# Performance work log

Hardware: AMD Instinct MI355X
Metric: run time of the kernel (lower is better)

The kernel has to match this reference:

```python
import jax, jax.numpy as jnp
import numpy as np

NUM_HEADS = 2
POOL_K = 256
REPEAT = 20


def setup_inputs() -> dict:
    key = jax.random.key(0)
    k1, k2, k3 = jax.random.split(key, 3)
    C = 6144
    d = C // NUM_HEADS                      # 3072
    N = REPEAT * (d // POOL_K)              # 240, required by Pq add
    x = jax.random.normal(k1, (N, C), dtype=jnp.float32)
    w_qkv = jax.random.normal(k2, (3 * C, C), dtype=jnp.float32) * 0.02
    w_proj = jax.random.normal(k3, (C, C), dtype=jnp.float32) * 0.02
    b_proj = jnp.zeros((C,), dtype=jnp.float32)
    return {"x": x, "w_qkv": w_qkv, "w_proj": w_proj, "b_proj": b_proj}


def reference(x, w_qkv, w_proj, b_proj):
    N, C = x.shape
    H = NUM_HEADS
    d = C // H
    scale = d ** -0.5
    # qkv: (N, 3C) -> (N, 3, H, d) -> (3, H, N, d)
    qkv = (x @ w_qkv.T).reshape(N, 3, H, d).transpose(1, 2, 0, 3)
    q, k, v = qkv[0], qkv[1], qkv[2]        # each (H, N, d)
    # MaxPool1d(256) over last dim, then tile x20 along last dim -> (H, N, N)
    Pq = q.reshape(H, N, d // POOL_K, POOL_K).max(axis=-1)
    Pq = jnp.tile(Pq, (1, 1, REPEAT))       # (H, N, N)
    attn = jnp.einsum('hnd,hmd->hnm', q, k) * scale + 0.1 * Pq
    attn = jax.nn.softmax(attn, axis=-1)
    out = jnp.einsum('hnm,hmd->hnd', attn, v)    # (H, N, d)
    out = out.transpose(1, 0, 2).reshape(N, C)
    return out @ w_proj.T + b_proj
```

## Files before the change

kernel.cpp:

```cpp
#include <hip/hip_runtime.h>
#include <hip/hip_bf16.h>

#define NN 240
#define CC 6144
#define DD 3072
#define C3 18432
#define HH 2

typedef __attribute__((ext_vector_type(8))) short bf16x8;
typedef __attribute__((ext_vector_type(4))) float f32x4;
typedef unsigned short ushort_t;

static __device__ __forceinline__ unsigned short f2bf(float f) {
    __hip_bfloat16 h = __float2bfloat16(f);
    return __builtin_bit_cast(unsigned short, h);
}

#define GLDS16(g, l) __builtin_amdgcn_global_load_lds( \
    (const __attribute__((address_space(1))) void*)(g), \
    (__attribute__((address_space(3))) void*)(l), 16, 0, 0)

__global__ __launch_bounds__(512, 4)
void gemm_v6(const ushort_t* __restrict__ Ab, int lda, long long sAz,
             const float* __restrict__ B, int ldb, long long sBz,
             const float* __restrict__ bias,
             float* __restrict__ C0, long long sC0z,
             float* __restrict__ CP, long long sCPz,
             int ldc, int N, int Kc, int KS,
             ushort_t* __restrict__ Qb) {
    __shared__ ushort_t sA[2][256 * 64];
    __shared__ ushort_t sB[2][32 * 64];

    const int zc = blockIdx.z;
    const int z = zc / KS, kc = zc % KS;
    const ushort_t* Abase = Ab + (size_t)z * sAz + (size_t)kc * Kc;
    const float*    Bbase = B  + (size_t)z * sBz + (size_t)kc * Kc;
    float* Cw = (kc == 0) ? (C0 + (size_t)z * sC0z)
                          : (CP + (size_t)(z * (KS - 1) + kc - 1) * sCPz);

    const int n0 = blockIdx.x * 32;
    const int tid = threadIdx.x, lane = tid & 63, wid = tid >> 6;
    const int wm = wid >> 1, wn = wid & 1;
    const int l16 = lane & 15, lk = lane >> 4;

    const int arow = wid * 32 + (lane >> 3);
    const ushort_t* ap = Abase + (size_t)arow * lda
                         + ((lane & 7) ^ ((lane >> 3) & 7)) * 8;

    const int brow = tid >> 4, bq = tid & 15;
    int brow_c = n0 + brow; if (brow_c > N - 1) brow_c = N - 1;
    const float* bp = Bbase + (size_t)brow_c * ldb + bq * 4;
    const int bws = brow * 128 + ((((bq >> 1) ^ (brow & 7)) << 4) + (bq & 1) * 8);

    const int nt = Kc / 64;
    f32x4 acc[4] = {};

    auto ISSUE_A = [&](int t, int par) {
        const ushort_t* a = ap + (size_t)t * 64;
#pragma unroll
        for (int i = 0; i < 4; ++i)
            GLDS16(a + (size_t)i * 8 * lda, &sA[par][(wid * 4 + i) * 512]);
    };
    auto LOAD_B = [&](int t) {
        return *(const float4*)(bp + (size_t)t * 64);
    };
    auto WRITE_B = [&](int par, float4 g) {
        ushort4 u;
        u.x = f2bf(g.x); u.y = f2bf(g.y); u.z = f2bf(g.z); u.w = f2bf(g.w);
        *(ushort4*)(reinterpret_cast<char*>(&sB[par][0]) + bws) = u;
    };
    auto MFMA_PH = [&](int cur) {
        const char* As = (const char*)sA[cur];
        const char* Bs = (const char*)sB[cur];
#pragma unroll
        for (int ks = 0; ks < 2; ++ks) {
            bf16x8 af[4], bf1;
#pragma unroll
            for (int mt = 0; mt < 4; ++mt) {
                int row = wm * 64 + mt * 16 + l16;
                int boff = row * 128 + (((ks * 4 + lk) * 16) ^ ((row & 7) << 4));
                af[mt] = *(const bf16x8*)(As + boff);
            }
            {
                int row = wn * 16 + l16;
                int boff = row * 128 + (((ks * 4 + lk) * 16) ^ ((row & 7) << 4));
                bf1 = *(const bf16x8*)(Bs + boff);
            }
            __builtin_amdgcn_s_setprio(1);
#pragma unroll
            for (int mt = 0; mt < 4; ++mt)
                acc[mt] = __builtin_amdgcn_mfma_f32_16x16x32_bf16(
                    af[mt], bf1, acc[mt], 0, 0, 0);
            __builtin_amdgcn_s_setprio(0);
        }
    };

    float4 e, o;

    ISSUE_A(0, 0);
    e = LOAD_B(0);
    o = (nt > 1) ? LOAD_B(1) : e;
    asm volatile("s_waitcnt vmcnt(1)" ::: "memory");
    __builtin_amdgcn_sched_barrier(0);
    WRITE_B(0, e);
    asm volatile("s_waitcnt lgkmcnt(0)" ::: "memory");
    __builtin_amdgcn_s_barrier();

    auto STEP = [&](int t, float4& w, float4& r) {
        int ta = t + 1 < nt ? t + 1 : nt - 1;
        int tb = t + 2 < nt ? t + 2 : nt - 1;
        ISSUE_A(ta, (t + 1) & 1);
        w = LOAD_B(tb);
        __builtin_amdgcn_sched_barrier(0);
        asm volatile("s_waitcnt vmcnt(6)" ::: "memory");
        __builtin_amdgcn_sched_barrier(0);
        MFMA_PH(t & 1);
        __builtin_amdgcn_sched_barrier(0);
        asm volatile("s_waitcnt vmcnt(5)" ::: "memory");
        __builtin_amdgcn_sched_barrier(0);
        WRITE_B((t + 1) & 1, r);
        asm volatile("s_waitcnt lgkmcnt(0)" ::: "memory");
        __builtin_amdgcn_s_barrier();
    };

    for (int t = 0; t < nt; t += 2) {
        STEP(t,     e, o);
        STEP(t + 1, o, e);
    }

#pragma unroll
    for (int mt = 0; mt < 4; ++mt) {
#pragma unroll
        for (int j = 0; j < 4; ++j) {
            int grow = wm * 64 + mt * 16 + lk * 4 + j;
            if (grow < NN) {
                int gcol = n0 + wn * 16 + l16;
                if (gcol < N) {
                    float v = acc[mt][j];
                    if (kc == 0 && bias) v += bias[gcol];
                    Cw[(size_t)grow * ldc + gcol] = v;
                    if (Qb && gcol < CC)
                        Qb[(size_t)grow * CC + gcol] = f2bf(v);
                }
            }
        }
    }
}

__global__ __launch_bounds__(256)
void convert_kernel(const float* __restrict__ x, ushort_t* __restrict__ xb) {
    int id = blockIdx.x * 256 + threadIdx.x;
    int row = id / 768, c8 = id % 768;
    bf16x8 o = {};
    if (row < NN) {
        const float* p = x + (size_t)row * CC + c8 * 8;
        float4 a = *(const float4*)p, b = *(const float4*)(p + 4);
        o[0] = (short)f2bf(a.x); o[1] = (short)f2bf(a.y);
        o[2] = (short)f2bf(a.z); o[3] = (short)f2bf(a.w);
        o[4] = (short)f2bf(b.x); o[5] = (short)f2bf(b.y);
        o[6] = (short)f2bf(b.z); o[7] = (short)f2bf(b.w);
    }
    *(bf16x8*)(xb + (size_t)row * CC + c8 * 8) = o;
}

__global__ __launch_bounds__(256)
void reduce_proj(float4* __restrict__ o4, const float4* __restrict__ p4,
                 long long s4) {
    int i = blockIdx.x * 256 + threadIdx.x;
    float4 a = o4[i];
#pragma unroll
    for (int k = 0; k < 2; ++k) {
        float4 b = p4[(size_t)k * s4 + i];
        a.x += b.x; a.y += b.y; a.z += b.z; a.w += b.w;
    }
    o4[i] = a;
}

__global__ __launch_bounds__(256)
void qmax_kernel(const float* __restrict__ qkv, float* __restrict__ qmax) {
    int idx = blockIdx.x * 4 + (threadIdx.x >> 6);
    int lane = threadIdx.x & 63;
    int c = idx % 12;
    int r = idx / 12;
    int n = r % NN, h = r / NN;
    const float* p = qkv + (size_t)n * C3 + h * DD + c * 256 + lane * 4;
    float4 f = *(const float4*)p;
    float m = fmaxf(fmaxf(f.x, f.y), fmaxf(f.z, f.w));
#pragma unroll
    for (int off = 32; off >= 1; off >>= 1)
        m = fmaxf(m, __shfl_xor(m, off));
    if (lane == 0) qmax[idx] = m;
}

__global__ __launch_bounds__(256)
void softmax_kernel(float* __restrict__ attn, const float* __restrict__ gpart,
                    int ksm1, const float* __restrict__ qmax) {
    int r = blockIdx.x * 4 + (threadIdx.x >> 6);
    int lane = threadIdx.x & 63;
    int z = r / NN, n = r % NN;
    float* row = attn + (size_t)r * NN;
    const float* qm = qmax + r * 12;
    const float scale = 0.0180421959f;
    float v[4];
    float mx = -1e30f;
#pragma unroll
    for (int i = 0; i < 4; ++i) {
        int m = lane + 64 * i;
        v[i] = -1e30f;
        if (m < NN) {
            float s = row[m];
            for (int kc = 0; kc < ksm1; ++kc)
                s += gpart[(size_t)(z * ksm1 + kc) * (NN * NN)
                           + (size_t)n * NN + m];
            v[i] = s * scale + 0.1f * qm[m % 12];
        }
        mx = fmaxf(mx, v[i]);
    }
#pragma unroll
    for (int off = 32; off >= 1; off >>= 1)
        mx = fmaxf(mx, __shfl_xor(mx, off));
    float s = 0.f;
#pragma unroll
    for (int i = 0; i < 4; ++i) {
        v[i] = __expf(v[i] - mx);
        s += v[i];
    }
#pragma unroll
    for (int off = 32; off >= 1; off >>= 1)
        s += __shfl_xor(s, off);
    float inv = 1.0f / s;
#pragma unroll
    for (int i = 0; i < 4; ++i) {
        int m = lane + 64 * i;
        if (m < NN) row[m] = v[i] * inv;
    }
}

__global__ __launch_bounds__(256)
void pv_kernel(const float* __restrict__ attn, const float* __restrict__ qkv,
               ushort_t* __restrict__ preb) {
    const int h = blockIdx.z;
    const int n0 = blockIdx.y * 16;
    const int dd0 = blockIdx.x * 256;
    __shared__ float s_attn[16 * NN];
    for (int i = threadIdx.x; i < 16 * NN; i += 256)
        s_attn[i] = attn[(size_t)h * NN * NN + (n0 + i / NN) * NN + (i % NN)];
    __syncthreads();

    const float* vp = qkv + 2 * CC + h * DD + dd0 + threadIdx.x;
    float acc[16] = {};
    for (int m = 0; m < NN; m += 4) {
        float v0 = vp[(size_t)(m + 0) * C3];
        float v1 = vp[(size_t)(m + 1) * C3];
        float v2 = vp[(size_t)(m + 2) * C3];
        float v3 = vp[(size_t)(m + 3) * C3];
#pragma unroll
        for (int i = 0; i < 16; ++i) {
            float4 a = *(const float4*)&s_attn[i * NN + m];
            acc[i] += a.x * v0 + a.y * v1 + a.z * v2 + a.w * v3;
        }
    }
#pragma unroll
    for (int i = 0; i < 16; ++i)
        preb[(size_t)(n0 + i) * CC + h * DD + dd0 + threadIdx.x] =
            f2bf(acc[i]);
}

extern "C" void kernel_launch(void* const* d_in, const int* in_sizes, int n_in,
                              void* d_out, int out_size, void* d_ws, size_t ws_size,
                              hipStream_t stream) {
    const float* x      = (const float*)d_in[0];
    const float* w_qkv  = (const float*)d_in[1];
    const float* w_proj = (const float*)d_in[2];
    const float* b_proj = (const float*)d_in[3];
    float* out = (float*)d_out;

    const size_t f_qkv  = (size_t)NN * C3;
    const size_t f_attn = (size_t)HH * NN * NN;
    const size_t f_qmax = (size_t)HH * NN * 12;
    float* qkv   = (float*)d_ws;
    float* attn  = qkv + f_qkv;
    float* qmaxb = attn + f_attn;
    ushort_t* xb   = (ushort_t*)(qmaxb + f_qmax);
    ushort_t* qb   = xb + (size_t)256 * CC;
    ushort_t* preb = qb + (size_t)256 * CC;
    float* gpart = (float*)(preb + (size_t)256 * CC);

    convert_kernel<<<768, 256, 0, stream>>>(x, xb);

    gemm_v6<<<dim3(C3 / 32, 1, 1), 512, 0, stream>>>(
        xb, CC, 0LL, w_qkv, CC, 0LL, nullptr,
        qkv, 0LL, gpart, 0LL,
        C3, C3, CC, 1, qb);

    qmax_kernel<<<1440, 256, 0, stream>>>(qkv, qmaxb);

    gemm_v6<<<dim3(8, 1, HH * 24), 512, 0, stream>>>(
        qb, CC, (long long)DD,
        qkv + CC, C3, (long long)DD, nullptr,
        attn, (long long)(NN * NN), gpart, (long long)(NN * NN),
        NN, NN, DD / 24, 24, nullptr);

    softmax_kernel<<<120, 256, 0, stream>>>(attn, gpart, 23, qmaxb);

    pv_kernel<<<dim3(12, 15, HH), 256, 0, stream>>>(attn, qkv, preb);

    gemm_v6<<<dim3(CC / 32, 1, 3), 512, 0, stream>>>(
        preb, CC, 0LL, w_proj, CC, 0LL, b_proj,
        out, 0LL, gpart, (long long)((size_t)NN * CC),
        CC, CC, CC / 3, 3, nullptr);
    reduce_proj<<<1440, 256, 0, stream>>>((float4*)out, (const float4*)gpart,
        (long long)((size_t)NN * CC / 4));
}
```

Measured before the change: 424.9 us.

## Keep B operand in registers and widen GEMM tile to 64 columns

Replaces the 512-thread GEMM, which staged the fp32 weight tile through LDS after bf16 conversion, with a 256-thread kernel. Each wave now loads its own 16 weight columns straight into registers, converts them, and feeds them as the MFMA B fragment. Each wave covers all 256 rows (16 accumulators), so the A tile in LDS is reused across four waves per 64-column block. This removes the LDS writes and reads for B and one barrier per step, but raises register pressure, lowers occupancy, halves the grid and leaves an uncoalesced-ish strided B load.

```diff
diff --git a/kernel.cpp b/kernel.cpp
--- a/kernel.cpp
+++ b/kernel.cpp
@@ -20,8 +20,8 @@
     (const __attribute__((address_space(1))) void*)(g), \
     (__attribute__((address_space(3))) void*)(l), 16, 0, 0)
 
-__global__ __launch_bounds__(512, 4)
-void gemm_v6(const ushort_t* __restrict__ Ab, int lda, long long sAz,
+__global__ __launch_bounds__(256, 2)
+void gemm_rs(const ushort_t* __restrict__ Ab, int lda, long long sAz,
              const float* __restrict__ B, int ldb, long long sBz,
              const float* __restrict__ bias,
              float* __restrict__ C0, long long sC0z,
@@ -29,7 +29,6 @@
              int ldc, int N, int Kc, int KS,
              ushort_t* __restrict__ Qb) {
     __shared__ ushort_t sA[2][256 * 64];
-    __shared__ ushort_t sB[2][32 * 64];
 
     const int zc = blockIdx.z;
     const int z = zc / KS, kc = zc % KS;
@@ -38,103 +37,88 @@
     float* Cw = (kc == 0) ? (C0 + (size_t)z * sC0z)
                           : (CP + (size_t)(z * (KS - 1) + kc - 1) * sCPz);
 
-    const int n0 = blockIdx.x * 32;
+    const int n0 = blockIdx.x * 64;
     const int tid = threadIdx.x, lane = tid & 63, wid = tid >> 6;
-    const int wm = wid >> 1, wn = wid & 1;
     const int l16 = lane & 15, lk = lane >> 4;
 
-    const int arow = wid * 32 + (lane >> 3);
-    const ushort_t* ap = Abase + (size_t)arow * lda
+    const ushort_t* ap = Abase + (size_t)(wid * 64 + (lane >> 3)) * lda
                          + ((lane & 7) ^ ((lane >> 3) & 7)) * 8;
 
-    const int brow = tid >> 4, bq = tid & 15;
-    int brow_c = n0 + brow; if (brow_c > N - 1) brow_c = N - 1;
-    const float* bp = Bbase + (size_t)brow_c * ldb + bq * 4;
-    const int bws = brow * 128 + ((((bq >> 1) ^ (brow & 7)) << 4) + (bq & 1) * 8);
+    int colc = n0 + wid * 16 + l16; if (colc > N - 1) colc = N - 1;
+    const float* bp = Bbase + (size_t)colc * ldb + lk * 8;
 
     const int nt = Kc / 64;
-    f32x4 acc[4] = {};
-
-    auto ISSUE_A = [&](int t, int par) {
-        const ushort_t* a = ap + (size_t)t * 64;
-#pragma unroll
-        for (int i = 0; i < 4; ++i)
-            GLDS16(a + (size_t)i * 8 * lda, &sA[par][(wid * 4 + i) * 512]);
-    };
-    auto LOAD_B = [&](int t) {
-        return *(const float4*)(bp + (size_t)t * 64);
-    };
-    auto WRITE_B = [&](int par, float4 g) {
-        ushort4 u;
-        u.x = f2bf(g.x); u.y = f2bf(g.y); u.z = f2bf(g.z); u.w = f2bf(g.w);
-        *(ushort4*)(reinterpret_cast<char*>(&sB[par][0]) + bws) = u;
-    };
-    auto MFMA_PH = [&](int cur) {
-        const char* As = (const char*)sA[cur];
-        const char* Bs = (const char*)sB[cur];
-#pragma unroll
-        for (int ks = 0; ks < 2; ++ks) {
-            bf16x8 af[4], bf1;
-#pragma unroll
-            for (int mt = 0; mt < 4; ++mt) {
-                int row = wm * 64 + mt * 16 + l16;
-                int boff = row * 128 + (((ks * 4 + lk) * 16) ^ ((row & 7) << 4));
-                af[mt] = *(const bf16x8*)(As + boff);
-            }
-            {
-                int row = wn * 16 + l16;
-                int boff = row * 128 + (((ks * 4 + lk) * 16) ^ ((row & 7) << 4));
-                bf1 = *(const bf16x8*)(Bs + boff);
-            }
-            __builtin_amdgcn_s_setprio(1);
-#pragma unroll
-            for (int mt = 0; mt < 4; ++mt)
-                acc[mt] = __builtin_amdgcn_mfma_f32_16x16x32_bf16(
-                    af[mt], bf1, acc[mt], 0, 0, 0);
-            __builtin_amdgcn_s_setprio(0);
-        }
-    };
-
-    float4 e, o;
+    f32x4 acc[16] = {};
+
+    auto ISSUE_A = [&](int u, int par) {
+        const ushort_t* a = ap + (size_t)u * 64;
+        ushort_t* d = &sA[par][wid * 8 * 512];
+#pragma unroll
+        for (int i = 0; i < 8; ++i)
+            GLDS16(a + (size_t)i * 8 * lda, d + i * 512);
+    };
+    auto LOAD_B4 = [&](int u, float4& b0, float4& b1, float4& b2, float4& b3) {
+        const float* p = bp + (size_t)u * 64;
+        b0 = *(const float4*)p;
+        b1 = *(const float4*)(p + 4);
+        b2 = *(const float4*)(p + 32);
+        b3 = *(const float4*)(p + 36);
+    };
+    auto PHASE = [&](int buf, int ph, float4 g0, float4 g1) {
+        bf16x8 bfr;
+        bfr[0] = (short)f2bf(g0.x); bfr[1] = (short)f2bf(g0.y);
+        bfr[2] = (short)f2bf(g0.z); bfr[3] = (short)f2bf(g0.w);
+        bfr[4] = (short)f2bf(g1.x); bfr[5] = (short)f2bf(g1.y);
+        bfr[6] = (short)f2bf(g1.z); bfr[7] = (short)f2bf(g1.w);
+        const char* As = (const char*)sA[buf];
+        __builtin_amdgcn_s_setprio(1);
+#pragma unroll
+        for (int mt = 0; mt < 16; ++mt) {
+            int row = mt * 16 + l16;
+            int boff = row * 128 + (((ph * 4 + lk) * 16) ^ ((row & 7) << 4));
+            bf16x8 af = *(const bf16x8*)(As + boff);
+            acc[mt] = __builtin_amdgcn_mfma_f32_16x16x32_bf16(
+                af, bfr, acc[mt], 0, 0, 0);
+        }
+        __builtin_amdgcn_s_setprio(0);
+    };
+
+    float4 e0, e1, e2, e3, o0, o1, o2, o3;
 
     ISSUE_A(0, 0);
-    e = LOAD_B(0);
-    o = (nt > 1) ? LOAD_B(1) : e;
-    asm volatile("s_waitcnt vmcnt(1)" ::: "memory");
+    LOAD_B4(0, e0, e1, e2, e3);
+    LOAD_B4(nt > 1 ? 1 : 0, o0, o1, o2, o3);
     __builtin_amdgcn_sched_barrier(0);
-    WRITE_B(0, e);
-    asm volatile("s_waitcnt lgkmcnt(0)" ::: "memory");
-    __builtin_amdgcn_s_barrier();
-
-    auto STEP = [&](int t, float4& w, float4& r) {
-        int ta = t + 1 < nt ? t + 1 : nt - 1;
-        int tb = t + 2 < nt ? t + 2 : nt - 1;
-        ISSUE_A(ta, (t + 1) & 1);
-        w = LOAD_B(tb);
-        __builtin_amdgcn_sched_barrier(0);
-        asm volatile("s_waitcnt vmcnt(6)" ::: "memory");
-        __builtin_amdgcn_sched_barrier(0);
-        MFMA_PH(t & 1);
-        __builtin_amdgcn_sched_barrier(0);
-        asm volatile("s_waitcnt vmcnt(5)" ::: "memory");
-        __builtin_amdgcn_sched_barrier(0);
-        WRITE_B((t + 1) & 1, r);
-        asm volatile("s_waitcnt lgkmcnt(0)" ::: "memory");
+
+    auto STEP = [&](int t,
+                    float4& r0, float4& r1, float4& r2, float4& r3,
+                    float4& w0, float4& w1, float4& w2, float4& w3) {
+        asm volatile("s_waitcnt vmcnt(4)" ::: "memory");
         __builtin_amdgcn_s_barrier();
+        __builtin_amdgcn_sched_barrier(0);
+        int ua = t + 1 < nt ? t + 1 : nt - 1;
+        ISSUE_A(ua, (t + 1) & 1);
+        __builtin_amdgcn_sched_barrier(0);
+        PHASE(t & 1, 0, r0, r1);
+        PHASE(t & 1, 1, r2, r3);
+        __builtin_amdgcn_sched_barrier(0);
+        int ub = t + 2 < nt ? t + 2 : nt - 1;
+        LOAD_B4(ub, w0, w1, w2, w3);
+        __builtin_amdgcn_sched_barrier(0);
     };
 
     for (int t = 0; t < nt; t += 2) {
-        STEP(t,     e, o);
-        STEP(t + 1, o, e);
-    }
-
-#pragma unroll
-    for (int mt = 0; mt < 4; ++mt) {
+        STEP(t,     e0, e1, e2, e3, e0, e1, e2, e3);
+        STEP(t + 1, o0, o1, o2, o3, o0, o1, o2, o3);
+    }
+
+#pragma unroll
+    for (int mt = 0; mt < 16; ++mt) {
 #pragma unroll
         for (int j = 0; j < 4; ++j) {
-            int grow = wm * 64 + mt * 16 + lk * 4 + j;
+            int grow = mt * 16 + lk * 4 + j;
             if (grow < NN) {
-                int gcol = n0 + wn * 16 + l16;
+                int gcol = n0 + wid * 16 + l16;
                 if (gcol < N) {
                     float v = acc[mt][j];
                     if (kc == 0 && bias) v += bias[gcol];
@@ -288,14 +272,14 @@
 
     convert_kernel<<<768, 256, 0, stream>>>(x, xb);
 
-    gemm_v6<<<dim3(C3 / 32, 1, 1), 512, 0, stream>>>(
+    gemm_rs<<<dim3(C3 / 64, 1, 1), 256, 0, stream>>>(
         xb, CC, 0LL, w_qkv, CC, 0LL, nullptr,
         qkv, 0LL, gpart, 0LL,
         C3, C3, CC, 1, qb);
 
     qmax_kernel<<<1440, 256, 0, stream>>>(qkv, qmaxb);
 
-    gemm_v6<<<dim3(8, 1, HH * 24), 512, 0, stream>>>(
+    gemm_rs<<<dim3(4, 1, HH * 24), 256, 0, stream>>>(
         qb, CC, (long long)DD,
         qkv + CC, C3, (long long)DD, nullptr,
         attn, (long long)(NN * NN), gpart, (long long)(NN * NN),
@@ -305,7 +289,7 @@
 
     pv_kernel<<<dim3(12, 15, HH), 256, 0, stream>>>(attn, qkv, preb);
 
-    gemm_v6<<<dim3(CC / 32, 1, 3), 512, 0, stream>>>(
+    gemm_rs<<<dim3(CC / 64, 1, 3), 256, 0, stream>>>(
         preb, CC, 0LL, w_proj, CC, 0LL, b_proj,
         out, 0LL, gpart, (long long)((size_t)NN * CC),
         CC, CC, CC / 3, 3, nullptr);
```

Result: faster. 404.7 us (-4.8%).
